# Kernel tuning notes

Hardware: AMD Instinct MI355X
Metric: run time of the kernel (lower is better)

## Reference

```python
import jax, jax.numpy as jnp
import numpy as np

MOL_SIZE = 64      # points per molecule (all molecules equal-size -> block-diagonal attn)
NUM_HEADS = 8
CUTOFF = 8.0
NUM_RBF = 32
LN_EPS = 1e-5


def setup_inputs() -> dict:
    key = jax.random.key(0)
    ks = jax.random.split(key, 6)
    B, K, hidden = 1024, MOL_SIZE, 512
    H = NUM_HEADS
    N = B * K
    h = jax.random.normal(ks[0], (N, hidden), jnp.float32)
    pos = jax.random.normal(ks[1], (N, 3), jnp.float32) * 3.0  # spread so dists hit RBF centers
    batch = jnp.repeat(jnp.arange(B, dtype=jnp.int32), K)
    s = lambda fin: 1.0 / np.sqrt(fin)
    centers = jnp.linspace(0.0, CUTOFF, NUM_RBF).astype(jnp.float32)  # RBFEncoder buffer
    w_rbf = jax.random.normal(ks[2], (NUM_RBF, H), jnp.float32) * s(NUM_RBF)
    b_rbf = jnp.zeros((H,), jnp.float32)
    w_qkv = jax.random.normal(ks[3], (hidden, 3 * hidden), jnp.float32) * s(hidden)
    b_qkv = jnp.zeros((3 * hidden,), jnp.float32)
    w_out = jax.random.normal(ks[4], (hidden, hidden), jnp.float32) * s(hidden)
    b_out = jnp.zeros((hidden,), jnp.float32)
    gamma = jnp.ones((hidden,), jnp.float32)
    beta = jnp.zeros((hidden,), jnp.float32)
    return {"h": h, "pos": pos, "batch": batch, "centers": centers,
            "w_rbf": w_rbf, "b_rbf": b_rbf, "w_qkv": w_qkv, "b_qkv": b_qkv,
            "w_out": w_out, "b_out": b_out, "gamma": gamma, "beta": beta}


def reference(h, pos, batch, centers, w_rbf, b_rbf, w_qkv, b_qkv, w_out, b_out, gamma, beta):
    N, hidden = h.shape
    K = MOL_SIZE
    B = N // K
    H = NUM_HEADS
    D = hidden // H
    width = (CUTOFF / NUM_RBF) ** 2
    scale = D ** -0.5

    # equal-size contiguous molecules -> reshape equals per-molecule loop
    hb = h.reshape(B, K, hidden)
    pb = pos.reshape(B, K, 3)

    qkv = hb @ w_qkv + b_qkv                      # [B,K,3*hidden]
    q, k, v = jnp.split(qkv, 3, axis=-1)
    q = q.reshape(B, K, H, D)
    k = k.reshape(B, K, H, D)
    v = v.reshape(B, K, H, D)

    diff = pb[:, :, None, :] - pb[:, None, :, :]  # [B,K,K,3]
    dist = jnp.sqrt(jnp.maximum(jnp.sum(diff * diff, axis=-1), 1e-12))  # torch.cdist
    rbf = jnp.exp(-((dist[..., None] - centers) ** 2) / width)          # [B,K,K,R]
    bias = jnp.transpose(rbf @ w_rbf + b_rbf, (0, 3, 1, 2))             # [B,H,K,K]

    attn = jnp.einsum('bkhd,bjhd->bhkj', q, k) * scale + bias
    attn = jax.nn.softmax(attn, axis=-1)
    agg = jnp.einsum('bhkj,bjhd->bkhd', attn, v).reshape(B, K, hidden)
    out = agg @ w_out + b_out

    y = hb + out
    mu = jnp.mean(y, axis=-1, keepdims=True)
    var = jnp.var(y, axis=-1, keepdims=True)
    y = (y - mu) / jnp.sqrt(var + LN_EPS) * gamma + beta
    return y.reshape(N, hidden)
```

## Files before the change

### kernel.cpp

```cpp
#include <hip/hip_runtime.h>
#include <hip/hip_bf16.h>


#define HID 512
#define TBL 512
#define DMAX 12.0f

typedef __attribute__((ext_vector_type(4))) float f32x4;
typedef __attribute__((ext_vector_type(8))) short bhalf8;

__device__ __forceinline__ short f2bf(float f) {
    union { float f; unsigned u; } x; x.f = f;
    unsigned u = x.u;
    unsigned r = (u + 0x7FFFu + ((u >> 16) & 1u)) >> 16;
    return (short)r;
}

__device__ __forceinline__ void gld_lds16(const void* g, void* l) {
    __builtin_amdgcn_global_load_lds((const __attribute__((address_space(1))) void*)g,
                                     (__attribute__((address_space(3))) void*)l, 16, 0, 0);
}

__global__ __launch_bounds__(256) void k_prep_w(const float* __restrict__ w_qkv,
                                                const float* __restrict__ w_out,
                                                short* __restrict__ wqT,
                                                short* __restrict__ woT) {
    __shared__ short tile[64][68];
    const int t = threadIdx.x;
    int bt = blockIdx.x;
    const float* src; short* dst; int sld, tk, tc, swz;
    if (bt < 192) { src = w_qkv; dst = wqT; sld = 1536; tk = bt & 7; tc = bt >> 3; swz = 1; }
    else { int b2 = bt - 192; src = w_out; dst = woT; sld = 512; tk = b2 & 7; tc = b2 >> 3; swz = 0; }
#pragma unroll
    for (int p = 0; p < 4; ++p) {
        int s = t + 256 * p;
        int r = s >> 4, sg = s & 15;
        const float4 v = *(const float4*)(src + (tk * 64 + r) * sld + tc * 64 + sg * 4);
        tile[r][sg * 4 + 0] = f2bf(v.x);
        tile[r][sg * 4 + 1] = f2bf(v.y);
        tile[r][sg * 4 + 2] = f2bf(v.z);
        tile[r][sg * 4 + 3] = f2bf(v.w);
    }
    __syncthreads();
#pragma unroll
    for (int p = 0; p < 16; ++p) {
        int o = t + 256 * p;
        int c = o >> 6, k = o & 63;
        int kk = swz ? (k ^ ((c & 7) << 3)) : k;
        dst[(tc * 64 + c) * 512 + tk * 64 + kk] = tile[k][c];
    }
}

__global__ __launch_bounds__(256) void k_prep_tbl(const float* __restrict__ centers,
                                                  const float* __restrict__ w_rbf,
                                                  const float* __restrict__ b_rbf,
                                                  float* __restrict__ tbl) {
    int idx = blockIdx.x * 256 + threadIdx.x;
    int hh = idx >> 9, i = idx & (TBL - 1);
    float d = (float)i * (DMAX / (float)(TBL - 1));
    float s = b_rbf[hh];
    const float invw = 1.0f / 0.0625f;
#pragma unroll 4
    for (int r = 0; r < 32; ++r) {
        float tt = d - centers[r];
        s += w_rbf[r * 8 + hh] * expf(-(tt * tt) * invw);
    }
    tbl[idx] = s;
}

__global__ __launch_bounds__(256) void k_prep_h(const float* __restrict__ h,
                                                short* __restrict__ hbf,
                                                int molbase) {
    size_t i = ((size_t)blockIdx.x * 256 + threadIdx.x) * 8;
    const float* src = h + (size_t)molbase * 64 * HID + i;
    float4 a = *(const float4*)src;
    float4 b = *(const float4*)(src + 4);
    short s8[8];
    s8[0] = f2bf(a.x); s8[1] = f2bf(a.y); s8[2] = f2bf(a.z); s8[3] = f2bf(a.w);
    s8[4] = f2bf(b.x); s8[5] = f2bf(b.y); s8[6] = f2bf(b.z); s8[7] = f2bf(b.w);
    int row = (int)(i >> 9);
    size_t o = i ^ (size_t)((row & 7) << 3);
    *(int4*)(hbf + o) = *(int4*)s8;
}

__global__ __launch_bounds__(512) void k_qkv(const short* __restrict__ hbf,
                                             const float* __restrict__ b_qkv,
                                             const short* __restrict__ wqT,
                                             short* __restrict__ qkvb) {
    __shared__ __align__(16) short As[128 * 64];
    __shared__ __align__(16) short Bs[256 * 64];
    const int t = threadIdx.x;
    const int lane = t & 63, wave = t >> 6;
    const int l16 = lane & 15, g = lane >> 4;
    const int wrow = wave >> 2, wcol = wave & 3;

    int wg = blockIdx.x;
    wg = (wg & 7) * 192 + (wg >> 3);
    const int bx = wg & 255, by = wg >> 8;
    const int R0l = bx * 128;
    const int C0 = by * 256;

    f32x4 acc[4][4];
#pragma unroll
    for (int i = 0; i < 4; ++i)
#pragma unroll
        for (int j = 0; j < 4; ++j) acc[i][j] = (f32x4){0.f, 0.f, 0.f, 0.f};

    const int lrow = lane >> 3, lslot = lane & 7;
    const int axor = (l16 & 7) << 3;

    for (int kc = 0; kc < 8; ++kc) {
        const int kb = kc * 64;
#pragma unroll
        for (int j = 0; j < 2; ++j) {
            int row = wave * 16 + j * 8 + lrow;
            gld_lds16(hbf + (size_t)(R0l + row) * HID + kb + lslot * 8,
                      (char*)As + wave * 2048 + j * 1024 + lane * 16);
        }
#pragma unroll
        for (int j = 0; j < 4; ++j) {
            int row = wave * 32 + j * 8 + lrow;
            gld_lds16(wqT + (size_t)(C0 + row) * HID + kb + lslot * 8,
                      (char*)Bs + wave * 4096 + j * 1024 + lane * 16);
        }
        __syncthreads();
#pragma unroll
        for (int kk = 0; kk < 2; ++kk) {
            const int cs = (kk * 32 + g * 8) ^ axor;
            bhalf8 af[4], bf[4];
#pragma unroll
            for (int mt = 0; mt < 4; ++mt)
                af[mt] = *(const bhalf8*)(&As[(wrow * 64 + mt * 16 + l16) * 64 + cs]);
#pragma unroll
            for (int nt = 0; nt < 4; ++nt)
                bf[nt] = *(const bhalf8*)(&Bs[(wcol * 64 + nt * 16 + l16) * 64 + cs]);
#pragma unroll
            for (int mt = 0; mt < 4; ++mt)
#pragma unroll
                for (int nt = 0; nt < 4; ++nt)
                    acc[mt][nt] = __builtin_amdgcn_mfma_f32_16x16x32_bf16(
                        af[mt], bf[nt], acc[mt][nt], 0, 0, 0);
        }
        __syncthreads();
    }

    const int sec = C0 >> 9;
    const float mul = (sec == 0) ? 0.125f : 1.0f;
#pragma unroll
    for (int nt = 0; nt < 4; ++nt) {
        int c = C0 + wcol * 64 + nt * 16 + l16;
        float bv = b_qkv[c];
        int head = (c >> 6) & 7, d = c & 63;
#pragma unroll
        for (int mt = 0; mt < 4; ++mt) {
            int rowl = R0l + wrow * 64 + mt * 16 + g * 4;
            int mol_local = rowl >> 6;
            int rloc = rowl & 63;
            short* panel = qkvb + (size_t)((mol_local * 3 + sec) * 8 + head) * 4096;
            if (sec == 2) {
                short4 s4;
                s4.x = f2bf(acc[mt][nt][0] + bv);
                s4.y = f2bf(acc[mt][nt][1] + bv);
                s4.z = f2bf(acc[mt][nt][2] + bv);
                s4.w = f2bf(acc[mt][nt][3] + bv);
                *(short4*)(panel + d * 64 + rloc) = s4;
            } else {
#pragma unroll
                for (int r = 0; r < 4; ++r)
                    panel[(rloc + r) * 64 + d] = f2bf((acc[mt][nt][r] + bv) * mul);
            }
        }
    }
}

__global__ __launch_bounds__(512) void k_fused(const short* __restrict__ qkvb,
                                               const float* __restrict__ pos,
                                               const float* __restrict__ tbl,
                                               const float* __restrict__ h,
                                               const short* __restrict__ woT,
                                               const float* __restrict__ b_out,
                                               const float* __restrict__ gamma,
                                               const float* __restrict__ beta,
                                               float* __restrict__ out,
                                               int molbase) {
    __shared__ __align__(16) short uP[8 * 4096];
    __shared__ float s_tbl[8 * 516];
    __shared__ float s_dc[64 * 66];
    __shared__ float s_px[64], s_py[64], s_pz[64];
    __shared__ float red[64 * 16];
    __shared__ float mr[64 * 2];

    const int t = threadIdx.x;
    const int wave = t >> 6, lane = t & 63;
    const int l16 = lane & 15, g = lane >> 4;
    const int mol_local = blockIdx.x;
    const int rowbase = (molbase + mol_local) * 64;
    const float tscale = (float)(TBL - 1) / DMAX;

    for (int i = t; i < 8 * TBL; i += 512)
        s_tbl[(i >> 9) * 516 + (i & (TBL - 1))] = tbl[i];
    if (t < 64) {
        s_px[t] = pos[(rowbase + t) * 3 + 0];
        s_py[t] = pos[(rowbase + t) * 3 + 1];
        s_pz[t] = pos[(rowbase + t) * 3 + 2];
    }
    __syncthreads();

    {
        int row = t >> 3, c0 = (t & 7) * 8;
        float rx = s_px[row], ry = s_py[row], rz = s_pz[row];
#pragma unroll
        for (int j = 0; j < 8; ++j) {
            int col = c0 + j;
            float dx = rx - s_px[col], dy = ry - s_py[col], dz = rz - s_pz[col];
            float dd = fmaf(dx, dx, fmaf(dy, dy, dz * dz));
            float dist = sqrtf(fmaxf(dd, 1e-12f));
            s_dc[row * 66 + col] = fminf(dist, DMAX) * tscale;
        }
    }
    __syncthreads();

    const short* qp = qkvb + ((size_t)(mol_local * 3 + 0) * 8 + wave) * 4096;
    const short* kp = qkvb + ((size_t)(mol_local * 3 + 1) * 8 + wave) * 4096;
    const short* vt = qkvb + ((size_t)(mol_local * 3 + 2) * 8 + wave) * 4096;

    f32x4 sacc[4][4];
#pragma unroll
    for (int i = 0; i < 4; ++i)
#pragma unroll
        for (int j = 0; j < 4; ++j) sacc[i][j] = (f32x4){0.f, 0.f, 0.f, 0.f};
#pragma unroll
    for (int kk = 0; kk < 2; ++kk) {
        bhalf8 qa[4], kb[4];
#pragma unroll
        for (int mt = 0; mt < 4; ++mt)
            qa[mt] = *(const bhalf8*)(qp + (mt * 16 + l16) * 64 + kk * 32 + g * 8);
#pragma unroll
        for (int nt = 0; nt < 4; ++nt)
            kb[nt] = *(const bhalf8*)(kp + (nt * 16 + l16) * 64 + kk * 32 + g * 8);
#pragma unroll
        for (int mt = 0; mt < 4; ++mt)
#pragma unroll
            for (int nt = 0; nt < 4; ++nt)
                sacc[mt][nt] = __builtin_amdgcn_mfma_f32_16x16x32_bf16(
                    qa[mt], kb[nt], sacc[mt][nt], 0, 0, 0);
    }

    const float* T = s_tbl + wave * 516;
#pragma unroll
    for (int nt = 0; nt < 4; ++nt) {
        int col = nt * 16 + l16;
#pragma unroll
        for (int mt = 0; mt < 4; ++mt) {
#pragma unroll
            for (int r = 0; r < 4; ++r) {
                int row = mt * 16 + g * 4 + r;
                float u = s_dc[row * 66 + col];
                int i = (int)u; if (i > TBL - 2) i = TBL - 2;
                float fr = u - (float)i;
                float t0 = T[i];
                sacc[mt][nt][r] += fmaf(fr, T[i + 1] - t0, t0);
            }
        }
    }

    float inv[4][4];
    short* Pw = uP + wave * 4096;
#pragma unroll
    for (int mt = 0; mt < 4; ++mt) {
#pragma unroll
        for (int r = 0; r < 4; ++r) {
            float m = fmaxf(fmaxf(sacc[mt][0][r], sacc[mt][1][r]),
                            fmaxf(sacc[mt][2][r], sacc[mt][3][r]));
#pragma unroll
            for (int off = 1; off < 16; off <<= 1) m = fmaxf(m, __shfl_xor(m, off, 64));
            float e[4], ssum = 0.f;
#pragma unroll
            for (int nt = 0; nt < 4; ++nt) { e[nt] = __expf(sacc[mt][nt][r] - m); ssum += e[nt]; }
#pragma unroll
            for (int off = 1; off < 16; off <<= 1) ssum += __shfl_xor(ssum, off, 64);
            inv[mt][r] = 1.0f / ssum;
            int row = mt * 16 + g * 4 + r;
            int rho = row & 7;
#pragma unroll
            for (int nt = 0; nt < 4; ++nt) {
                int c = nt * 16 + l16;
                Pw[row * 64 + (((c >> 3) ^ rho) << 3) + (c & 7)] = f2bf(e[nt]);
            }
        }
    }

    f32x4 oacc[4][4];
#pragma unroll
    for (int i = 0; i < 4; ++i)
#pragma unroll
        for (int j = 0; j < 4; ++j) oacc[i][j] = (f32x4){0.f, 0.f, 0.f, 0.f};
#pragma unroll
    for (int kk = 0; kk < 2; ++kk) {
        bhalf8 pa[4], vb[4];
#pragma unroll
        for (int mt = 0; mt < 4; ++mt)
            pa[mt] = *(const bhalf8*)(Pw + (mt * 16 + l16) * 64 +
                                      (((kk * 4 + g) ^ (l16 & 7)) << 3));
#pragma unroll
        for (int nt = 0; nt < 4; ++nt)
            vb[nt] = *(const bhalf8*)(vt + (nt * 16 + l16) * 64 + kk * 32 + g * 8);
#pragma unroll
        for (int mt = 0; mt < 4; ++mt)
#pragma unroll
            for (int nt = 0; nt < 4; ++nt)
                oacc[mt][nt] = __builtin_amdgcn_mfma_f32_16x16x32_bf16(
                    pa[mt], vb[nt], oacc[mt][nt], 0, 0, 0);
    }
#pragma unroll
    for (int mt = 0; mt < 4; ++mt)
#pragma unroll
        for (int nt = 0; nt < 4; ++nt)
#pragma unroll
            for (int r = 0; r < 4; ++r) oacc[mt][nt][r] *= inv[mt][r];

    __syncthreads();

#pragma unroll
    for (int mt = 0; mt < 4; ++mt) {
#pragma unroll
        for (int r = 0; r < 4; ++r) {
            int row = mt * 16 + g * 4 + r;
            int rho = row & 7;
#pragma unroll
            for (int nt = 0; nt < 4; ++nt) {
                int c = wave * 64 + nt * 16 + l16;
                uP[row * 512 + (((c >> 3) ^ rho) << 3) + (c & 7)] = f2bf(oacc[mt][nt][r]);
            }
        }
    }
    __syncthreads();

    f32x4 pacc[4][4];
#pragma unroll
    for (int i = 0; i < 4; ++i)
#pragma unroll
        for (int j = 0; j < 4; ++j) pacc[i][j] = (f32x4){0.f, 0.f, 0.f, 0.f};
#pragma unroll 4
    for (int kc = 0; kc < 16; ++kc) {
        bhalf8 af[4], bw[4];
#pragma unroll
        for (int mt = 0; mt < 4; ++mt)
            af[mt] = *(const bhalf8*)(uP + (mt * 16 + l16) * 512 +
                                      (((kc * 4 + g) ^ (l16 & 7)) << 3));
#pragma unroll
        for (int nt = 0; nt < 4; ++nt)
            bw[nt] = *(const bhalf8*)(woT + (size_t)(wave * 64 + nt * 16 + l16) * HID +
                                      kc * 32 + g * 8);
#pragma unroll
        for (int mt = 0; mt < 4; ++mt)
#pragma unroll
            for (int nt = 0; nt < 4; ++nt)
                pacc[mt][nt] = __builtin_amdgcn_mfma_f32_16x16x32_bf16(
                    af[mt], bw[nt], pacc[mt][nt], 0, 0, 0);
    }

#pragma unroll
    for (int mt = 0; mt < 4; ++mt) {
#pragma unroll
        for (int r = 0; r < 4; ++r) {
            int row = mt * 16 + g * 4 + r;
            float rs = 0.f, rq = 0.f;
#pragma unroll
            for (int nt = 0; nt < 4; ++nt) {
                int col = wave * 64 + nt * 16 + l16;
                float v = pacc[mt][nt][r] + b_out[col] +
                          h[(size_t)(rowbase + row) * HID + col];
                pacc[mt][nt][r] = v;
                rs += v;
                rq = fmaf(v, v, rq);
            }
#pragma unroll
            for (int off = 1; off < 16; off <<= 1) {
                rs += __shfl_xor(rs, off, 64);
                rq += __shfl_xor(rq, off, 64);
            }
            if (l16 == 0) {
                red[row * 16 + wave * 2 + 0] = rs;
                red[row * 16 + wave * 2 + 1] = rq;
            }
        }
    }
    __syncthreads();
    if (t < 64) {
        float s = 0.f, q = 0.f;
#pragma unroll
        for (int w = 0; w < 8; ++w) {
            s += red[t * 16 + w * 2 + 0];
            q += red[t * 16 + w * 2 + 1];
        }
        float mean = s * (1.0f / 512.0f);
        float var = q * (1.0f / 512.0f) - mean * mean;
        mr[t * 2 + 0] = mean;
        mr[t * 2 + 1] = rsqrtf(var + 1e-5f);
    }
    __syncthreads();
#pragma unroll
    for (int mt = 0; mt < 4; ++mt) {
#pragma unroll
        for (int r = 0; r < 4; ++r) {
            int row = mt * 16 + g * 4 + r;
            float mean = mr[row * 2 + 0], rstd = mr[row * 2 + 1];
#pragma unroll
            for (int nt = 0; nt < 4; ++nt) {
                int col = wave * 64 + nt * 16 + l16;
                out[(size_t)(rowbase + row) * HID + col] =
                    fmaf((pacc[mt][nt][r] - mean) * rstd, gamma[col], beta[col]);
            }
        }
    }
}

extern "C" void kernel_launch(void* const* d_in, const int* in_sizes, int n_in,
                              void* d_out, int out_size, void* d_ws, size_t ws_size,
                              hipStream_t stream) {
    (void)in_sizes; (void)n_in; (void)out_size; (void)ws_size;
    const float* h       = (const float*)d_in[0];
    const float* pos     = (const float*)d_in[1];
    const float* centers = (const float*)d_in[3];
    const float* w_rbf   = (const float*)d_in[4];
    const float* b_rbf   = (const float*)d_in[5];
    const float* w_qkv   = (const float*)d_in[6];
    const float* b_qkv   = (const float*)d_in[7];
    const float* w_out   = (const float*)d_in[8];
    const float* b_out   = (const float*)d_in[9];
    const float* gamma   = (const float*)d_in[10];
    const float* beta    = (const float*)d_in[11];
    float* out = (float*)d_out;

    char* ws = (char*)d_ws;
    short* wqT  = (short*)ws;
    short* woT  = (short*)(ws + 1572864);
    float* tbl  = (float*)(ws + 2097152);
    short* hbf  = (short*)(ws + 2162688);
    short* qkvb = (short*)(ws + 35717120);

    k_prep_w<<<256, 256, 0, stream>>>(w_qkv, w_out, wqT, woT);
    k_prep_tbl<<<16, 256, 0, stream>>>(centers, w_rbf, b_rbf, tbl);
    for (int half = 0; half < 2; ++half) {
        int molbase = half * 512;
        k_prep_h<<<8192, 256, 0, stream>>>(h, hbf, molbase);
        k_qkv<<<1536, 512, 0, stream>>>(hbf, b_qkv, wqT, qkvb);
        k_fused<<<512, 512, 0, stream>>>(qkvb, pos, tbl, h, woT, b_out,
                                         gamma, beta, out, molbase);
    }
}
```

Measured before the change: 398.3 us.

## Use 1024 threads per molecule block in fused attention kernel

The fused attention/out-projection/LayerNorm kernel now runs 16 waves per molecule instead of 8. Each head is split across two waves, each taking 32 query rows, and the output projection is split into 2 row halves by 8 column slices. This halves the per-wave accumulator and register footprint and adds parallelism within a block. In exchange it doubles K/V and weight fragment loads per output and allows fewer concurrent blocks per CU at the larger block size.

```diff
diff --git a/kernel.cpp b/kernel.cpp
--- a/kernel.cpp
+++ b/kernel.cpp
@@ -173,16 +173,16 @@
     }
 }
 
-__global__ __launch_bounds__(512) void k_fused(const short* __restrict__ qkvb,
-                                               const float* __restrict__ pos,
-                                               const float* __restrict__ tbl,
-                                               const float* __restrict__ h,
-                                               const short* __restrict__ woT,
-                                               const float* __restrict__ b_out,
-                                               const float* __restrict__ gamma,
-                                               const float* __restrict__ beta,
-                                               float* __restrict__ out,
-                                               int molbase) {
+__global__ __launch_bounds__(1024) void k_fused(const short* __restrict__ qkvb,
+                                                const float* __restrict__ pos,
+                                                const float* __restrict__ tbl,
+                                                const float* __restrict__ h,
+                                                const short* __restrict__ woT,
+                                                const float* __restrict__ b_out,
+                                                const float* __restrict__ gamma,
+                                                const float* __restrict__ beta,
+                                                float* __restrict__ out,
+                                                int molbase) {
     __shared__ __align__(16) short uP[8 * 4096];
     __shared__ float s_tbl[8 * 516];
     __shared__ float s_dc[64 * 66];
@@ -193,11 +193,12 @@
     const int t = threadIdx.x;
     const int wave = t >> 6, lane = t & 63;
     const int l16 = lane & 15, g = lane >> 4;
+    const int head = wave >> 1, sub = wave & 1;
     const int mol_local = blockIdx.x;
     const int rowbase = (molbase + mol_local) * 64;
     const float tscale = (float)(TBL - 1) / DMAX;
 
-    for (int i = t; i < 8 * TBL; i += 512)
+    for (int i = t; i < 8 * TBL; i += 1024)
         s_tbl[(i >> 9) * 516 + (i & (TBL - 1))] = tbl[i];
     if (t < 64) {
         s_px[t] = pos[(rowbase + t) * 3 + 0];
@@ -207,10 +208,10 @@
     __syncthreads();
 
     {
-        int row = t >> 3, c0 = (t & 7) * 8;
+        int row = t >> 4, c0 = (t & 15) * 4;
         float rx = s_px[row], ry = s_py[row], rz = s_pz[row];
 #pragma unroll
-        for (int j = 0; j < 8; ++j) {
+        for (int j = 0; j < 4; ++j) {
             int col = c0 + j;
             float dx = rx - s_px[col], dy = ry - s_py[col], dz = rz - s_pz[col];
             float dd = fmaf(dx, dx, fmaf(dy, dy, dz * dz));
@@ -220,41 +221,41 @@
     }
     __syncthreads();
 
-    const short* qp = qkvb + ((size_t)(mol_local * 3 + 0) * 8 + wave) * 4096;
-    const short* kp = qkvb + ((size_t)(mol_local * 3 + 1) * 8 + wave) * 4096;
-    const short* vt = qkvb + ((size_t)(mol_local * 3 + 2) * 8 + wave) * 4096;
-
-    f32x4 sacc[4][4];
-#pragma unroll
-    for (int i = 0; i < 4; ++i)
+    const short* qp = qkvb + ((size_t)(mol_local * 3 + 0) * 8 + head) * 4096;
+    const short* kp = qkvb + ((size_t)(mol_local * 3 + 1) * 8 + head) * 4096;
+    const short* vt = qkvb + ((size_t)(mol_local * 3 + 2) * 8 + head) * 4096;
+
+    f32x4 sacc[2][4];
+#pragma unroll
+    for (int i = 0; i < 2; ++i)
 #pragma unroll
         for (int j = 0; j < 4; ++j) sacc[i][j] = (f32x4){0.f, 0.f, 0.f, 0.f};
 #pragma unroll
     for (int kk = 0; kk < 2; ++kk) {
-        bhalf8 qa[4], kb[4];
-#pragma unroll
-        for (int mt = 0; mt < 4; ++mt)
-            qa[mt] = *(const bhalf8*)(qp + (mt * 16 + l16) * 64 + kk * 32 + g * 8);
+        bhalf8 qa[2], kb[4];
+#pragma unroll
+        for (int mt = 0; mt < 2; ++mt)
+            qa[mt] = *(const bhalf8*)(qp + (sub * 32 + mt * 16 + l16) * 64 + kk * 32 + g * 8);
 #pragma unroll
         for (int nt = 0; nt < 4; ++nt)
             kb[nt] = *(const bhalf8*)(kp + (nt * 16 + l16) * 64 + kk * 32 + g * 8);
 #pragma unroll
-        for (int mt = 0; mt < 4; ++mt)
+        for (int mt = 0; mt < 2; ++mt)
 #pragma unroll
             for (int nt = 0; nt < 4; ++nt)
                 sacc[mt][nt] = __builtin_amdgcn_mfma_f32_16x16x32_bf16(
                     qa[mt], kb[nt], sacc[mt][nt], 0, 0, 0);
     }
 
-    const float* T = s_tbl + wave * 516;
+    const float* T = s_tbl + head * 516;
 #pragma unroll
     for (int nt = 0; nt < 4; ++nt) {
         int col = nt * 16 + l16;
 #pragma unroll
-        for (int mt = 0; mt < 4; ++mt) {
+        for (int mt = 0; mt < 2; ++mt) {
 #pragma unroll
             for (int r = 0; r < 4; ++r) {
-                int row = mt * 16 + g * 4 + r;
+                int row = sub * 32 + mt * 16 + g * 4 + r;
                 float u = s_dc[row * 66 + col];
                 int i = (int)u; if (i > TBL - 2) i = TBL - 2;
                 float fr = u - (float)i;
@@ -264,10 +265,10 @@
         }
     }
 
-    float inv[4][4];
-    short* Pw = uP + wave * 4096;
-#pragma unroll
-    for (int mt = 0; mt < 4; ++mt) {
+    float inv[2][4];
+    short* Pw = uP + head * 4096;
+#pragma unroll
+    for (int mt = 0; mt < 2; ++mt) {
 #pragma unroll
         for (int r = 0; r < 4; ++r) {
             float m = fmaxf(fmaxf(sacc[mt][0][r], sacc[mt][1][r]),
@@ -280,7 +281,7 @@
 #pragma unroll
             for (int off = 1; off < 16; off <<= 1) ssum += __shfl_xor(ssum, off, 64);
             inv[mt][r] = 1.0f / ssum;
-            int row = mt * 16 + g * 4 + r;
+            int row = sub * 32 + mt * 16 + g * 4 + r;
             int rho = row & 7;
 #pragma unroll
             for (int nt = 0; nt < 4; ++nt) {
@@ -290,30 +291,31 @@
         }
     }
 
-    f32x4 oacc[4][4];
-#pragma unroll
-    for (int i = 0; i < 4; ++i)
+    f32x4 oacc[2][4];
+#pragma unroll
+    for (int i = 0; i < 2; ++i)
 #pragma unroll
         for (int j = 0; j < 4; ++j) oacc[i][j] = (f32x4){0.f, 0.f, 0.f, 0.f};
 #pragma unroll
     for (int kk = 0; kk < 2; ++kk) {
-        bhalf8 pa[4], vb[4];
-#pragma unroll
-        for (int mt = 0; mt < 4; ++mt)
-            pa[mt] = *(const bhalf8*)(Pw + (mt * 16 + l16) * 64 +
-                                      (((kk * 4 + g) ^ (l16 & 7)) << 3));
+        bhalf8 pa[2], vb[4];
+#pragma unroll
+        for (int mt = 0; mt < 2; ++mt) {
+            int prow = sub * 32 + mt * 16 + l16;
+            pa[mt] = *(const bhalf8*)(Pw + prow * 64 + (((kk * 4 + g) ^ (prow & 7)) << 3));
+        }
 #pragma unroll
         for (int nt = 0; nt < 4; ++nt)
             vb[nt] = *(const bhalf8*)(vt + (nt * 16 + l16) * 64 + kk * 32 + g * 8);
 #pragma unroll
-        for (int mt = 0; mt < 4; ++mt)
+        for (int mt = 0; mt < 2; ++mt)
 #pragma unroll
             for (int nt = 0; nt < 4; ++nt)
                 oacc[mt][nt] = __builtin_amdgcn_mfma_f32_16x16x32_bf16(
                     pa[mt], vb[nt], oacc[mt][nt], 0, 0, 0);
     }
 #pragma unroll
-    for (int mt = 0; mt < 4; ++mt)
+    for (int mt = 0; mt < 2; ++mt)
 #pragma unroll
         for (int nt = 0; nt < 4; ++nt)
 #pragma unroll
@@ -322,56 +324,58 @@
     __syncthreads();
 
 #pragma unroll
-    for (int mt = 0; mt < 4; ++mt) {
+    for (int mt = 0; mt < 2; ++mt) {
 #pragma unroll
         for (int r = 0; r < 4; ++r) {
-            int row = mt * 16 + g * 4 + r;
+            int row = sub * 32 + mt * 16 + g * 4 + r;
             int rho = row & 7;
 #pragma unroll
             for (int nt = 0; nt < 4; ++nt) {
-                int c = wave * 64 + nt * 16 + l16;
+                int c = head * 64 + nt * 16 + l16;
                 uP[row * 512 + (((c >> 3) ^ rho) << 3) + (c & 7)] = f2bf(oacc[mt][nt][r]);
             }
         }
     }
     __syncthreads();
 
-    f32x4 pacc[4][4];
-#pragma unroll
-    for (int i = 0; i < 4; ++i)
+    const int wrow2 = wave >> 3, wcol8 = wave & 7;
+    f32x4 pacc[2][4];
+#pragma unroll
+    for (int i = 0; i < 2; ++i)
 #pragma unroll
         for (int j = 0; j < 4; ++j) pacc[i][j] = (f32x4){0.f, 0.f, 0.f, 0.f};
 #pragma unroll 4
     for (int kc = 0; kc < 16; ++kc) {
-        bhalf8 af[4], bw[4];
-#pragma unroll
-        for (int mt = 0; mt < 4; ++mt)
-            af[mt] = *(const bhalf8*)(uP + (mt * 16 + l16) * 512 +
-                                      (((kc * 4 + g) ^ (l16 & 7)) << 3));
+        bhalf8 af[2], bw[4];
+#pragma unroll
+        for (int pt = 0; pt < 2; ++pt) {
+            int rl = wrow2 * 32 + pt * 16 + l16;
+            af[pt] = *(const bhalf8*)(uP + rl * 512 + (((kc * 4 + g) ^ (rl & 7)) << 3));
+        }
 #pragma unroll
         for (int nt = 0; nt < 4; ++nt)
-            bw[nt] = *(const bhalf8*)(woT + (size_t)(wave * 64 + nt * 16 + l16) * HID +
+            bw[nt] = *(const bhalf8*)(woT + (size_t)(wcol8 * 64 + nt * 16 + l16) * HID +
                                       kc * 32 + g * 8);
 #pragma unroll
-        for (int mt = 0; mt < 4; ++mt)
+        for (int pt = 0; pt < 2; ++pt)
 #pragma unroll
             for (int nt = 0; nt < 4; ++nt)
-                pacc[mt][nt] = __builtin_amdgcn_mfma_f32_16x16x32_bf16(
-                    af[mt], bw[nt], pacc[mt][nt], 0, 0, 0);
-    }
-
-#pragma unroll
-    for (int mt = 0; mt < 4; ++mt) {
+                pacc[pt][nt] = __builtin_amdgcn_mfma_f32_16x16x32_bf16(
+                    af[pt], bw[nt], pacc[pt][nt], 0, 0, 0);
+    }
+
+#pragma unroll
+    for (int pt = 0; pt < 2; ++pt) {
 #pragma unroll
         for (int r = 0; r < 4; ++r) {
-            int row = mt * 16 + g * 4 + r;
+            int row = wrow2 * 32 + pt * 16 + g * 4 + r;
             float rs = 0.f, rq = 0.f;
 #pragma unroll
             for (int nt = 0; nt < 4; ++nt) {
-                int col = wave * 64 + nt * 16 + l16;
-                float v = pacc[mt][nt][r] + b_out[col] +
+                int col = wcol8 * 64 + nt * 16 + l16;
+                float v = pacc[pt][nt][r] + b_out[col] +
                           h[(size_t)(rowbase + row) * HID + col];
-                pacc[mt][nt][r] = v;
+                pacc[pt][nt][r] = v;
                 rs += v;
                 rq = fmaf(v, v, rq);
             }
@@ -381,8 +385,8 @@
                 rq += __shfl_xor(rq, off, 64);
             }
             if (l16 == 0) {
-                red[row * 16 + wave * 2 + 0] = rs;
-                red[row * 16 + wave * 2 + 1] = rq;
+                red[(row * 8 + wcol8) * 2 + 0] = rs;
+                red[(row * 8 + wcol8) * 2 + 1] = rq;
             }
         }
     }
@@ -391,8 +395,8 @@
         float s = 0.f, q = 0.f;
 #pragma unroll
         for (int w = 0; w < 8; ++w) {
-            s += red[t * 16 + w * 2 + 0];
-            q += red[t * 16 + w * 2 + 1];
+            s += red[(t * 8 + w) * 2 + 0];
+            q += red[(t * 8 + w) * 2 + 1];
         }
         float mean = s * (1.0f / 512.0f);
         float var = q * (1.0f / 512.0f) - mean * mean;
@@ -401,16 +405,16 @@
     }
     __syncthreads();
 #pragma unroll
-    for (int mt = 0; mt < 4; ++mt) {
+    for (int pt = 0; pt < 2; ++pt) {
 #pragma unroll
         for (int r = 0; r < 4; ++r) {
-            int row = mt * 16 + g * 4 + r;
+            int row = wrow2 * 32 + pt * 16 + g * 4 + r;
             float mean = mr[row * 2 + 0], rstd = mr[row * 2 + 1];
 #pragma unroll
             for (int nt = 0; nt < 4; ++nt) {
-                int col = wave * 64 + nt * 16 + l16;
+                int col = wcol8 * 64 + nt * 16 + l16;
                 out[(size_t)(rowbase + row) * HID + col] =
-                    fmaf((pacc[mt][nt][r] - mean) * rstd, gamma[col], beta[col]);
+                    fmaf((pacc[pt][nt][r] - mean) * rstd, gamma[col], beta[col]);
             }
         }
     }
@@ -446,7 +450,7 @@
         int molbase = half * 512;
         k_prep_h<<<8192, 256, 0, stream>>>(h, hbf, molbase);
         k_qkv<<<1536, 512, 0, stream>>>(hbf, b_qkv, wqT, qkvb);
-        k_fused<<<512, 512, 0, stream>>>(qkvb, pos, tbl, h, woT, b_out,
-                                         gamma, beta, out, molbase);
-    }
-}
+        k_fused<<<512, 1024, 0, stream>>>(qkvb, pos, tbl, h, woT, b_out,
+                                          gamma, beta, out, molbase);
+    }
+}
```

After: 428.0 us. 7.5% more time.

## Prefetch Wo and V fragments, read residual from bf16 copy early

Applied to the files above, without the earlier changes.

Hoists the V fragment loads ahead of the bias/softmax section and double-buffers the w_out fragment loads across the projection loop so global latency overlaps MFMA work. The fp32 residual read of h is replaced by an early gather from the bf16 (swizzled) staging copy produced for the QKV GEMM. This halves residual traffic and issues it before the projection GEMM, but it adds register pressure and drops the residual to bf16 precision.

```diff
diff --git a/kernel.cpp b/kernel.cpp
--- a/kernel.cpp
+++ b/kernel.cpp
@@ -14,6 +14,11 @@
     unsigned u = x.u;
     unsigned r = (u + 0x7FFFu + ((u >> 16) & 1u)) >> 16;
     return (short)r;
+}
+
+__device__ __forceinline__ float bf2f(unsigned short s) {
+    union { unsigned u; float f; } x; x.u = ((unsigned)s) << 16;
+    return x.f;
 }
 
 __device__ __forceinline__ void gld_lds16(const void* g, void* l) {
@@ -176,7 +181,7 @@
 __global__ __launch_bounds__(512) void k_fused(const short* __restrict__ qkvb,
                                                const float* __restrict__ pos,
                                                const float* __restrict__ tbl,
-                                               const float* __restrict__ h,
+                                               const short* __restrict__ hbfr,
                                                const short* __restrict__ woT,
                                                const float* __restrict__ b_out,
                                                const float* __restrict__ gamma,
@@ -246,6 +251,13 @@
                     qa[mt], kb[nt], sacc[mt][nt], 0, 0, 0);
     }
 
+    bhalf8 vb[2][4];
+#pragma unroll
+    for (int kk = 0; kk < 2; ++kk)
+#pragma unroll
+        for (int nt = 0; nt < 4; ++nt)
+            vb[kk][nt] = *(const bhalf8*)(vt + (nt * 16 + l16) * 64 + kk * 32 + g * 8);
+
     const float* T = s_tbl + wave * 516;
 #pragma unroll
     for (int nt = 0; nt < 4; ++nt) {
@@ -297,20 +309,17 @@
         for (int j = 0; j < 4; ++j) oacc[i][j] = (f32x4){0.f, 0.f, 0.f, 0.f};
 #pragma unroll
     for (int kk = 0; kk < 2; ++kk) {
-        bhalf8 pa[4], vb[4];
+        bhalf8 pa[4];
 #pragma unroll
         for (int mt = 0; mt < 4; ++mt)
             pa[mt] = *(const bhalf8*)(Pw + (mt * 16 + l16) * 64 +
                                       (((kk * 4 + g) ^ (l16 & 7)) << 3));
 #pragma unroll
-        for (int nt = 0; nt < 4; ++nt)
-            vb[nt] = *(const bhalf8*)(vt + (nt * 16 + l16) * 64 + kk * 32 + g * 8);
-#pragma unroll
         for (int mt = 0; mt < 4; ++mt)
 #pragma unroll
             for (int nt = 0; nt < 4; ++nt)
                 oacc[mt][nt] = __builtin_amdgcn_mfma_f32_16x16x32_bf16(
-                    pa[mt], vb[nt], oacc[mt][nt], 0, 0, 0);
+                    pa[mt], vb[kk][nt], oacc[mt][nt], 0, 0, 0);
     }
 #pragma unroll
     for (int mt = 0; mt < 4; ++mt)
@@ -336,28 +345,51 @@
     }
     __syncthreads();
 
+    unsigned short hres[4][4][4];
+#pragma unroll
+    for (int mt = 0; mt < 4; ++mt)
+#pragma unroll
+        for (int r = 0; r < 4; ++r) {
+            int row = mt * 16 + g * 4 + r;
+            size_t rbase = (size_t)(mol_local * 64 + row) * HID;
+            int sw = (row & 7) << 3;
+#pragma unroll
+            for (int nt = 0; nt < 4; ++nt) {
+                int col = wave * 64 + nt * 16 + l16;
+                hres[mt][r][nt] = *(const unsigned short*)(hbfr + rbase + (col ^ sw));
+            }
+        }
+
     f32x4 pacc[4][4];
 #pragma unroll
     for (int i = 0; i < 4; ++i)
 #pragma unroll
         for (int j = 0; j < 4; ++j) pacc[i][j] = (f32x4){0.f, 0.f, 0.f, 0.f};
-#pragma unroll 4
+    bhalf8 bwc[4], bwn[4];
+#pragma unroll
+    for (int nt = 0; nt < 4; ++nt)
+        bwc[nt] = *(const bhalf8*)(woT + (size_t)(wave * 64 + nt * 16 + l16) * HID + g * 8);
+#pragma unroll
     for (int kc = 0; kc < 16; ++kc) {
-        bhalf8 af[4], bw[4];
+        if (kc < 15) {
+#pragma unroll
+            for (int nt = 0; nt < 4; ++nt)
+                bwn[nt] = *(const bhalf8*)(woT + (size_t)(wave * 64 + nt * 16 + l16) * HID +
+                                           (kc + 1) * 32 + g * 8);
+        }
+        bhalf8 af[4];
 #pragma unroll
         for (int mt = 0; mt < 4; ++mt)
             af[mt] = *(const bhalf8*)(uP + (mt * 16 + l16) * 512 +
                                       (((kc * 4 + g) ^ (l16 & 7)) << 3));
 #pragma unroll
-        for (int nt = 0; nt < 4; ++nt)
-            bw[nt] = *(const bhalf8*)(woT + (size_t)(wave * 64 + nt * 16 + l16) * HID +
-                                      kc * 32 + g * 8);
-#pragma unroll
         for (int mt = 0; mt < 4; ++mt)
 #pragma unroll
             for (int nt = 0; nt < 4; ++nt)
                 pacc[mt][nt] = __builtin_amdgcn_mfma_f32_16x16x32_bf16(
-                    af[mt], bw[nt], pacc[mt][nt], 0, 0, 0);
+                    af[mt], bwc[nt], pacc[mt][nt], 0, 0, 0);
+#pragma unroll
+        for (int nt = 0; nt < 4; ++nt) bwc[nt] = bwn[nt];
     }
 
 #pragma unroll
@@ -369,8 +401,7 @@
 #pragma unroll
             for (int nt = 0; nt < 4; ++nt) {
                 int col = wave * 64 + nt * 16 + l16;
-                float v = pacc[mt][nt][r] + b_out[col] +
-                          h[(size_t)(rowbase + row) * HID + col];
+                float v = pacc[mt][nt][r] + b_out[col] + bf2f(hres[mt][r][nt]);
                 pacc[mt][nt][r] = v;
                 rs += v;
                 rq = fmaf(v, v, rq);
@@ -446,7 +477,7 @@
         int molbase = half * 512;
         k_prep_h<<<8192, 256, 0, stream>>>(h, hbf, molbase);
         k_qkv<<<1536, 512, 0, stream>>>(hbf, b_qkv, wqT, qkvb);
-        k_fused<<<512, 512, 0, stream>>>(qkvb, pos, tbl, h, woT, b_out,
+        k_fused<<<512, 512, 0, stream>>>(qkvb, pos, tbl, hbf, woT, b_out,
                                          gamma, beta, out, molbase);
     }
 }
```

Result: faster. 390.4 us (-2.0%).
